# Kernel tuning notes

Measured on AMD Instinct MI355X. Metric: run time of the kernel, lower is better.

The kernel has to match this reference:

```python
import jax, jax.numpy as jnp
import numpy as np

TAU = 0.1
EPS = 1e-8

def _l2norm(x, axis):
    # matches F.normalize: x / max(||x||, 1e-12)
    n = jnp.sqrt(jnp.sum(x * x, axis=axis, keepdims=True))
    return x / jnp.maximum(n, 1e-12)

def setup_inputs() -> dict:
    key = jax.random.key(0)
    k1, k2, k3 = jax.random.split(key, 3)
    B, D, K = 262144, 256, 64
    return {
        "features": jax.random.normal(k1, (B, D), dtype=jnp.float32),
        "prototypes": jax.random.normal(k2, (K, D), dtype=jnp.float32),
        "domain_labels": jax.random.randint(k3, (B,), 0, K, dtype=jnp.int64),
    }

def reference(features, prototypes, domain_labels):
    f = _l2norm(features, 1)            # (B, D)
    p = _l2norm(prototypes, 1)          # (K, D)
    sim = jnp.einsum('bd,kd->bk', f, p) / TAU   # (B, K)
    e = jnp.exp(sim)                    # (B, K)
    numerator = jnp.take_along_axis(e, domain_labels[:, None], axis=1)[:, 0]  # (B,)
    denominator = jnp.sum(e, axis=1)    # (B,)
    loss = -jnp.log((numerator + EPS) / (denominator + EPS) + EPS)
    return jnp.mean(loss)
```

## Files before the change

### kernel.cpp

```cpp
#include <hip/hip_runtime.h>
#include <stdint.h>

typedef __attribute__((ext_vector_type(8))) short short8;
typedef __attribute__((ext_vector_type(4))) float floatx4;

#define EPS 1e-8f
#define TAU 0.1f

__device__ __forceinline__ unsigned short f2bf(float f) {
  union { float f; unsigned u; } v; v.f = f;
  unsigned u = v.u;
  u += 0x7fffu + ((u >> 16) & 1u);
  return (unsigned short)(u >> 16);
}

__device__ __forceinline__ unsigned pack2_trunc(float lo, float hi) {
  union { float f; unsigned u; } a, b; a.f = lo; b.f = hi;
  return __builtin_amdgcn_perm(b.u, a.u, 0x07060302u);
}

__global__ void proto_prep(const float* __restrict__ protos,
                           unsigned short* __restrict__ pbf) {
  const int l = threadIdx.x & 63;
  const int w = threadIdx.x >> 6;
  const int row = blockIdx.x * 4 + w;
  float4 v = reinterpret_cast<const float4*>(protos)[row * 64 + l];
  float ss = v.x * v.x + v.y * v.y + v.z * v.z + v.w * v.w;
#pragma unroll
  for (int d = 1; d < 64; d <<= 1) ss += __shfl_xor(ss, d, 64);
  const float inv = 1.0f / fmaxf(sqrtf(ss), 1e-12f);
  ushort4 o;
  o.x = f2bf(v.x * inv); o.y = f2bf(v.y * inv);
  o.z = f2bf(v.z * inv); o.w = f2bf(v.w * inv);
  reinterpret_cast<ushort4*>(pbf)[row * 64 + l] = o;
}

__global__ __launch_bounds__(256, 4)
void protonce_main(const float* __restrict__ feat,
                   const unsigned short* __restrict__ pbf,
                   const int* __restrict__ labels,
                   float* __restrict__ partials) {
  const int tid = threadIdx.x;
  const int l = tid & 63;
  const int w = tid >> 6;
  const int n = l & 15;
  const int q = l >> 4;
  const long rowBase = (long)blockIdx.x * 64 + w * 16;

  const float* arow = feat + (rowBase + n) * 256 + q * 8;
  const unsigned short* bbase = pbf + n * 256 + q * 8;

  float4 avx[4], avy[4];
#pragma unroll
  for (int i = 0; i < 4; ++i) {
    avx[i] = *reinterpret_cast<const float4*>(arow + i * 32);
    avy[i] = *reinterpret_cast<const float4*>(arow + i * 32 + 4);
  }

  floatx4 acc[4] = {{0.f, 0.f, 0.f, 0.f}, {0.f, 0.f, 0.f, 0.f},
                    {0.f, 0.f, 0.f, 0.f}, {0.f, 0.f, 0.f, 0.f}};
  float ss = 0.f;

#pragma unroll
  for (int s = 0; s < 8; ++s) {
    float4 x = avx[s & 3], y = avy[s & 3];
    if (s < 4) {
      avx[s & 3] = *reinterpret_cast<const float4*>(arow + (s + 4) * 32);
      avy[s & 3] = *reinterpret_cast<const float4*>(arow + (s + 4) * 32 + 4);
    }
    ss += x.x * x.x + x.y * x.y + x.z * x.z + x.w * x.w +
          y.x * y.x + y.y * y.y + y.z * y.z + y.w * y.w;
    union { short8 s8; uint4 u4; } af;
    af.u4.x = pack2_trunc(x.x, x.y);
    af.u4.y = pack2_trunc(x.z, x.w);
    af.u4.z = pack2_trunc(y.x, y.y);
    af.u4.w = pack2_trunc(y.z, y.w);
#pragma unroll
    for (int t = 0; t < 4; ++t) {
      short8 bf = *reinterpret_cast<const short8*>(bbase + t * 4096 + s * 32);
      acc[t] = __builtin_amdgcn_mfma_f32_16x16x32_bf16(af.s8, bf, acc[t], 0, 0, 0);
    }
  }

  ss += __shfl_xor(ss, 16, 64);
  ss += __shfl_xor(ss, 32, 64);

  const int4 lv = *reinterpret_cast<const int4*>(labels + rowBase + q * 4);
  float lossAcc = 0.f;
#pragma unroll
  for (int r = 0; r < 4; ++r) {
    const int row = q * 4 + r;
    const float nrm = __shfl(ss, row, 64);
    const float sc = 1.0f / (fmaxf(sqrtf(nrm), 1e-12f) * TAU);
    const int lab = (r == 0) ? lv.x : (r == 1) ? lv.y : (r == 2) ? lv.z : lv.w;
    float den = 0.f, num = 0.f;
#pragma unroll
    for (int t = 0; t < 4; ++t) {
      const float e = __expf(acc[t][r] * sc);
      den += e;
      num += (t * 16 + n == lab) ? e : 0.f;
    }
#pragma unroll
    for (int d = 1; d < 16; d <<= 1) {
      den += __shfl_xor(den, d, 64);
      num += __shfl_xor(num, d, 64);
    }
    if (n == 0) lossAcc += -__logf((num + EPS) / (den + EPS) + EPS);
  }
  lossAcc += __shfl_xor(lossAcc, 16, 64);
  lossAcc += __shfl_xor(lossAcc, 32, 64);

  __shared__ float wsum[4];
  if (l == 0) wsum[w] = lossAcc;
  __syncthreads();
  if (tid == 0) partials[blockIdx.x] = wsum[0] + wsum[1] + wsum[2] + wsum[3];
}

__global__ void finalize_k(const float* __restrict__ partials, int nblocks,
                           float* __restrict__ out, float invB) {
  __shared__ float red[256];
  float s = 0.f;
  for (int i = threadIdx.x; i < nblocks; i += 256) s += partials[i];
  red[threadIdx.x] = s;
  __syncthreads();
#pragma unroll
  for (int d = 128; d > 0; d >>= 1) {
    if (threadIdx.x < d) red[threadIdx.x] += red[threadIdx.x + d];
    __syncthreads();
  }
  if (threadIdx.x == 0) out[0] = red[0] * invB;
}

extern "C" void kernel_launch(void* const* d_in, const int* in_sizes, int n_in,
                              void* d_out, int out_size, void* d_ws, size_t ws_size,
                              hipStream_t stream) {
  const float* feat = (const float*)d_in[0];
  const float* protos = (const float*)d_in[1];
  const int* labels = (const int*)d_in[2];
  float* out = (float*)d_out;
  const int Bn = in_sizes[0] / 256;
  const int nblocks = Bn / 64;
  unsigned short* pbf = (unsigned short*)d_ws;
  float* partials = (float*)((char*)d_ws + 64 * 256 * sizeof(unsigned short));

  hipLaunchKernelGGL(proto_prep, dim3(16), dim3(256), 0, stream, protos, pbf);
  hipLaunchKernelGGL(protonce_main, dim3(nblocks), dim3(256), 0, stream,
                     feat, pbf, labels, partials);
  hipLaunchKernelGGL(finalize_k, dim3(1), dim3(256), 0, stream, partials,
                     nblocks, out, 1.0f / (float)Bn);
}
```

Baseline: 377.4 us.

## Stage feature tiles through LDS with async copies and split prototype columns across waves

Each block now handles 32 rows. Feature rows are copied into padded LDS with global_load_lds async copies, replacing strided per-lane global float4 loads. The four waves form a 2x2 grid: each covers 16 rows by 32 prototypes and keeps its 32 prototype columns in registers. Partial denominators and numerators are combined through shared memory before the log. The goal is coalesced feature reads and fewer repeated prototype loads per MFMA, at the cost of twice as many blocks, two barriers, and 33KB of LDS per block, which may limit occupancy.

```diff
diff --git a/kernel.cpp b/kernel.cpp
--- a/kernel.cpp
+++ b/kernel.cpp
@@ -6,6 +6,7 @@
 
 #define EPS 1e-8f
 #define TAU 0.1f
+#define LROW 264
 
 __device__ __forceinline__ unsigned short f2bf(float f) {
   union { float f; unsigned u; } v; v.f = f;
@@ -17,6 +18,12 @@
 __device__ __forceinline__ unsigned pack2_trunc(float lo, float hi) {
   union { float f; unsigned u; } a, b; a.f = lo; b.f = hi;
   return __builtin_amdgcn_perm(b.u, a.u, 0x07060302u);
+}
+
+__device__ __forceinline__ void async_copy16(const void* g, void* l) {
+  __builtin_amdgcn_global_load_lds(
+      (__attribute__((address_space(1))) void*)g,
+      (__attribute__((address_space(3))) void*)l, 16, 0, 0);
 }
 
 __global__ void proto_prep(const float* __restrict__ protos,
@@ -40,34 +47,41 @@
                    const unsigned short* __restrict__ pbf,
                    const int* __restrict__ labels,
                    float* __restrict__ partials) {
+  __shared__ __align__(16) float At[32 * LROW];
+  __shared__ float dn_sm[2][32];
+  __shared__ float nm_sm[2][32];
+
   const int tid = threadIdx.x;
   const int l = tid & 63;
   const int w = tid >> 6;
+  const int mw = w & 1;
+  const int nw = w >> 1;
   const int n = l & 15;
   const int q = l >> 4;
-  const long rowBase = (long)blockIdx.x * 64 + w * 16;
+  const long rowBase = (long)blockIdx.x * 32;
 
-  const float* arow = feat + (rowBase + n) * 256 + q * 8;
-  const unsigned short* bbase = pbf + n * 256 + q * 8;
+  const float* srcw = feat + (rowBase + w * 8) * 256 + l * 4;
+#pragma unroll
+  for (int j = 0; j < 8; ++j)
+    async_copy16(srcw + j * 256, &At[(w * 8 + j) * LROW]);
 
-  float4 avx[4], avy[4];
+  const unsigned short* bbase = pbf + (nw * 32 + n) * 256 + q * 8;
+  short8 bv[16];
 #pragma unroll
-  for (int i = 0; i < 4; ++i) {
-    avx[i] = *reinterpret_cast<const float4*>(arow + i * 32);
-    avy[i] = *reinterpret_cast<const float4*>(arow + i * 32 + 4);
+  for (int s = 0; s < 8; ++s) {
+    bv[2 * s]     = *reinterpret_cast<const short8*>(bbase + s * 32);
+    bv[2 * s + 1] = *reinterpret_cast<const short8*>(bbase + 16 * 256 + s * 32);
   }
 
-  floatx4 acc[4] = {{0.f, 0.f, 0.f, 0.f}, {0.f, 0.f, 0.f, 0.f},
-                    {0.f, 0.f, 0.f, 0.f}, {0.f, 0.f, 0.f, 0.f}};
+  __syncthreads();
+
+  floatx4 acc0 = {0.f, 0.f, 0.f, 0.f}, acc1 = {0.f, 0.f, 0.f, 0.f};
   float ss = 0.f;
-
+  const float* arow = &At[(mw * 16 + n) * LROW + q * 8];
 #pragma unroll
   for (int s = 0; s < 8; ++s) {
-    float4 x = avx[s & 3], y = avy[s & 3];
-    if (s < 4) {
-      avx[s & 3] = *reinterpret_cast<const float4*>(arow + (s + 4) * 32);
-      avy[s & 3] = *reinterpret_cast<const float4*>(arow + (s + 4) * 32 + 4);
-    }
+    float4 x = *reinterpret_cast<const float4*>(arow + s * 32);
+    float4 y = *reinterpret_cast<const float4*>(arow + s * 32 + 4);
     ss += x.x * x.x + x.y * x.y + x.z * x.z + x.w * x.w +
           y.x * y.x + y.y * y.y + y.z * y.z + y.w * y.w;
     union { short8 s8; uint4 u4; } af;
@@ -75,45 +89,45 @@
     af.u4.y = pack2_trunc(x.z, x.w);
     af.u4.z = pack2_trunc(y.x, y.y);
     af.u4.w = pack2_trunc(y.z, y.w);
-#pragma unroll
-    for (int t = 0; t < 4; ++t) {
-      short8 bf = *reinterpret_cast<const short8*>(bbase + t * 4096 + s * 32);
-      acc[t] = __builtin_amdgcn_mfma_f32_16x16x32_bf16(af.s8, bf, acc[t], 0, 0, 0);
-    }
+    acc0 = __builtin_amdgcn_mfma_f32_16x16x32_bf16(af.s8, bv[2 * s],     acc0, 0, 0, 0);
+    acc1 = __builtin_amdgcn_mfma_f32_16x16x32_bf16(af.s8, bv[2 * s + 1], acc1, 0, 0, 0);
   }
-
   ss += __shfl_xor(ss, 16, 64);
   ss += __shfl_xor(ss, 32, 64);
 
-  const int4 lv = *reinterpret_cast<const int4*>(labels + rowBase + q * 4);
-  float lossAcc = 0.f;
+  const int4 lv = *reinterpret_cast<const int4*>(labels + rowBase + mw * 16 + q * 4);
 #pragma unroll
   for (int r = 0; r < 4; ++r) {
-    const int row = q * 4 + r;
-    const float nrm = __shfl(ss, row, 64);
+    const float nrm = __shfl(ss, q * 4 + r, 64);
     const float sc = 1.0f / (fmaxf(sqrtf(nrm), 1e-12f) * TAU);
     const int lab = (r == 0) ? lv.x : (r == 1) ? lv.y : (r == 2) ? lv.z : lv.w;
-    float den = 0.f, num = 0.f;
-#pragma unroll
-    for (int t = 0; t < 4; ++t) {
-      const float e = __expf(acc[t][r] * sc);
-      den += e;
-      num += (t * 16 + n == lab) ? e : 0.f;
-    }
+    const float e0 = __expf(acc0[r] * sc);
+    const float e1 = __expf(acc1[r] * sc);
+    float den = e0 + e1;
+    float num = (nw * 32 + n == lab ? e0 : 0.f) + (nw * 32 + 16 + n == lab ? e1 : 0.f);
 #pragma unroll
     for (int d = 1; d < 16; d <<= 1) {
       den += __shfl_xor(den, d, 64);
       num += __shfl_xor(num, d, 64);
     }
-    if (n == 0) lossAcc += -__logf((num + EPS) / (den + EPS) + EPS);
+    if (n == 0) {
+      dn_sm[nw][mw * 16 + q * 4 + r] = den;
+      nm_sm[nw][mw * 16 + q * 4 + r] = num;
+    }
   }
-  lossAcc += __shfl_xor(lossAcc, 16, 64);
-  lossAcc += __shfl_xor(lossAcc, 32, 64);
+  __syncthreads();
 
-  __shared__ float wsum[4];
-  if (l == 0) wsum[w] = lossAcc;
-  __syncthreads();
-  if (tid == 0) partials[blockIdx.x] = wsum[0] + wsum[1] + wsum[2] + wsum[3];
+  if (w == 0) {
+    float loss = 0.f;
+    if (l < 32) {
+      const float den = dn_sm[0][l] + dn_sm[1][l];
+      const float num = nm_sm[0][l] + nm_sm[1][l];
+      loss = -__logf((num + EPS) / (den + EPS) + EPS);
+    }
+#pragma unroll
+    for (int d = 1; d < 64; d <<= 1) loss += __shfl_xor(loss, d, 64);
+    if (l == 0) partials[blockIdx.x] = loss;
+  }
 }
 
 __global__ void finalize_k(const float* __restrict__ partials, int nblocks,
@@ -139,7 +153,7 @@
   const int* labels = (const int*)d_in[2];
   float* out = (float*)d_out;
   const int Bn = in_sizes[0] / 256;
-  const int nblocks = Bn / 64;
+  const int nblocks = Bn / 32;
   unsigned short* pbf = (unsigned short*)d_ws;
   float* partials = (float*)((char*)d_ws + 64 * 256 * sizeof(unsigned short));
 
```

Result: faster. 367.5 us (-2.6%).
